# Kernel tuning notes

Measured on AMD Instinct MI355X. Metric: run time of the kernel, lower is better.

Reference implementation:

```python
import jax, jax.numpy as jnp
import numpy as np

N = 8192       # paired user/item batch
D_IN = 10000   # interaction-vector length
H = 1024       # hidden width
E = 128        # shared embedding dim


def setup_inputs() -> dict:
    key = jax.random.key(0)
    ks = jax.random.split(key, 10)
    g = 5.0 / 3.0  # tanh gain used by the torch init

    def xavier(k, shape):
        fan_in, fan_out = shape
        std = g * np.sqrt(2.0 / (fan_in + fan_out))
        return jax.random.normal(k, shape, dtype=jnp.float32) * std

    return {
        "user_data": jax.random.normal(ks[0], (N, D_IN), dtype=jnp.float32),
        "item_data": jax.random.normal(ks[1], (N, D_IN), dtype=jnp.float32),
        "Wu1": xavier(ks[2], (D_IN, H)),
        "bu1": jnp.full((H,), 0.01, dtype=jnp.float32),
        "Wu2": xavier(ks[3], (H, E)),
        "bu2": jnp.full((E,), 0.01, dtype=jnp.float32),
        "Wi1": xavier(ks[4], (D_IN, H)),
        "bi1": jnp.full((H,), 0.01, dtype=jnp.float32),
        "Wi2": xavier(ks[5], (H, E)),
        "bi2": jnp.full((E,), 0.01, dtype=jnp.float32),
    }


def reference(user_data, item_data, Wu1, bu1, Wu2, bu2, Wi1, bi1, Wi2, bi2):
    # Encoders (dropout is identity at inference). PolyLinear: Linear -> ReLU -> Linear.
    p = jax.nn.relu(user_data @ Wu1 + bu1) @ Wu2 + bu2   # [N, E]
    q = jax.nn.relu(item_data @ Wi1 + bi1) @ Wi2 + bi2   # [N, E]
    # (p @ q.T).diag() == row-wise dot product; identical math, O(N*E) not O(N^2*E).
    return jnp.einsum("ne,ne->n", p, q)
```

## Files before the change

### kernel.cpp

```cpp
#include <hip/hip_runtime.h>
#include <hip/hip_bf16.h>
#include <stdint.h>

#define KP   10112
#define DIN  10000
#define NB   8192
#define HID  1024
#define EMB  128
#define NKT  313
#define NI   79

typedef __attribute__((ext_vector_type(8))) __bf16 bf16x8;
typedef __attribute__((ext_vector_type(4))) float  f32x4;
typedef __attribute__((ext_vector_type(4))) unsigned short ushort4v;

typedef const __attribute__((address_space(1))) void* gas_cp;
typedef __attribute__((address_space(3))) void* las_p;

__device__ __forceinline__ unsigned short f2bf(float f) {
    union { float f; unsigned u; } c; c.f = f;
    unsigned u = c.u;
    u += 0x7FFFu + ((u >> 16) & 1u);
    return (unsigned short)(u >> 16);
}

__global__ void conv_pad(const float* __restrict__ src, unsigned short* __restrict__ dst) {
    const int c4  = blockIdx.x * blockDim.x + threadIdx.x;
    const int row = blockIdx.y;
    if (c4 >= KP / 4) return;
    ushort4v o;
    if (c4 < DIN / 4) {
        float4 a = *(const float4*)(src + (size_t)row * DIN + (size_t)c4 * 4);
        o[0] = f2bf(a.x); o[1] = f2bf(a.y); o[2] = f2bf(a.z); o[3] = f2bf(a.w);
    } else {
        o[0] = o[1] = o[2] = o[3] = 0;
    }
    *(ushort4v*)(dst + (size_t)row * KP + (size_t)c4 * 4) = o;
}

__global__ void conv_transpose(const float* __restrict__ src, unsigned short* __restrict__ dst,
                               int K, int N, int Kp) {
    __shared__ float tile[64][33];
    const int tx = threadIdx.x & 31, ty = threadIdx.x >> 5;
    const int k0 = blockIdx.x * 64, n0 = blockIdx.y * 32;
#pragma unroll
    for (int j = 0; j < 8; ++j) {
        int k = k0 + ty + j * 8;
        tile[ty + j * 8][tx] = (k < K) ? src[(size_t)k * N + n0 + tx] : 0.0f;
    }
    __syncthreads();
#pragma unroll
    for (int j = 0; j < 4; ++j) {
        int n = n0 + ty + j * 8;
        unsigned short lo = f2bf(tile[2 * tx][ty + j * 8]);
        unsigned short hi = f2bf(tile[2 * tx + 1][ty + j * 8]);
        unsigned int packed = (unsigned int)lo | ((unsigned int)hi << 16);
        *(unsigned int*)(dst + (size_t)n * Kp + k0 + 2 * tx) = packed;
    }
}

#define DSR(d, ad, off) asm volatile("ds_read_b128 %0, %1 offset:" off : "=v"(d) : "v"(ad))
#define GATE(n) do { asm volatile("s_waitcnt lgkmcnt(" #n ")" ::: "memory"); \
                     __builtin_amdgcn_sched_barrier(0); } while (0)

__global__ __launch_bounds__(512, 2)
void gemm1_4p(const unsigned short* __restrict__ Abf,
              const unsigned short* __restrict__ W1t,
              const float* __restrict__ b1u, const float* __restrict__ b1i,
              unsigned short* __restrict__ H1) {
    __shared__ __align__(16) unsigned short lds_[81920];

    const int t  = threadIdx.x;
    const int lane = t & 63, wv = t >> 6;
    const int wm = wv >> 2, wn = wv & 3;
    const int rA = lane & 15, kg = lane >> 4;

    const int side = blockIdx.x >> 2, bn = blockIdx.x & 3, bm = blockIdx.y;

    const unsigned short* AbfS = Abf + (size_t)side * NB * KP;
    const unsigned short* W1tS = W1t + (size_t)side * HID * KP;
    const float* bias = side ? b1i : b1u;
    unsigned short* Cout = H1 + (size_t)side * NB * HID;

    const int rowSA = bm * 256 + (t >> 3);
    const int rowSB = bn * 256 + (t >> 3);
    const int kcl   = ((t & 7) ^ ((t >> 3) & 7)) * 8;

    const int xk0 = ((0 * 4 + kg) ^ (rA & 7)) * 8;
    const int xk1 = ((1 * 4 + kg) ^ (rA & 7)) * 8;

    const unsigned ldsB = (unsigned)(size_t)lds_;
    const unsigned aC0 = ldsB + wm * 16384 + rA * 128 + xk0 * 2;
    const unsigned aC1 = ldsB + wm * 16384 + rA * 128 + xk1 * 2;
    const unsigned bC0 = ldsB + 98304 + (wn >> 1) * 16384 + (wn & 1) * 8192 + rA * 128 + xk0 * 2;
    const unsigned bC1 = ldsB + 98304 + (wn >> 1) * 16384 + (wn & 1) * 8192 + rA * 128 + xk1 * 2;

    f32x4 acc[8][4] = {};
    bf16x8 a[4][2], b[4][2];

    auto stA = [&](int tile, int h, int buf) {
        const unsigned short* s = AbfS + (size_t)(rowSA + h * 128) * KP + tile * 64 + kcl;
        __builtin_amdgcn_global_load_lds((gas_cp)s, (las_p)(lds_ + buf * 16384 + h * 8192 + wv * 512), 16, 0, 0);
        __builtin_amdgcn_global_load_lds((gas_cp)(s + (size_t)64 * KP), (las_p)(lds_ + buf * 16384 + h * 8192 + 4096 + wv * 512), 16, 0, 0);
    };
    auto stB = [&](int tile, int h, int par) {
        const unsigned short* s = W1tS + (size_t)(rowSB + h * 128) * KP + tile * 64 + kcl;
        __builtin_amdgcn_global_load_lds((gas_cp)s, (las_p)(lds_ + 49152 + par * 16384 + h * 8192 + wv * 512), 16, 0, 0);
        __builtin_amdgcn_global_load_lds((gas_cp)(s + (size_t)64 * KP), (las_p)(lds_ + 49152 + par * 16384 + h * 8192 + 4096 + wv * 512), 16, 0, 0);
    };

    auto rdB01 = [&](int par) {
        unsigned b0 = bC0 + par * 32768, b1 = bC1 + par * 32768;
        DSR(b[0][0], b0, "0");    DSR(b[0][1], b1, "0");
        DSR(b[1][0], b0, "2048"); DSR(b[1][1], b1, "2048");
    };
    auto rdB23 = [&](int par) {
        unsigned b0 = bC0 + par * 32768 + 4096, b1 = bC1 + par * 32768 + 4096;
        DSR(b[2][0], b0, "0");    DSR(b[2][1], b1, "0");
        DSR(b[3][0], b0, "2048"); DSR(b[3][1], b1, "2048");
    };
    auto rdA4 = [&](int buf, int mq) {
        unsigned a0 = aC0 + buf * 32768 + mq * 8192, a1 = aC1 + buf * 32768 + mq * 8192;
        DSR(a[0][0], a0, "0");    DSR(a[0][1], a1, "0");
        DSR(a[1][0], a0, "2048"); DSR(a[1][1], a1, "2048");
        DSR(a[2][0], a0, "4096"); DSR(a[2][1], a1, "4096");
        DSR(a[3][0], a0, "6144"); DSR(a[3][1], a1, "6144");
    };
    auto mmj = [&](int mq, int j, int nq) {
        acc[mq*4+j][nq*2+0] = __builtin_amdgcn_mfma_f32_16x16x32_bf16(a[j][0], b[nq*2+0][0], acc[mq*4+j][nq*2+0], 0, 0, 0);
        acc[mq*4+j][nq*2+0] = __builtin_amdgcn_mfma_f32_16x16x32_bf16(a[j][1], b[nq*2+0][1], acc[mq*4+j][nq*2+0], 0, 0, 0);
        acc[mq*4+j][nq*2+1] = __builtin_amdgcn_mfma_f32_16x16x32_bf16(a[j][0], b[nq*2+1][0], acc[mq*4+j][nq*2+1], 0, 0, 0);
        acc[mq*4+j][nq*2+1] = __builtin_amdgcn_mfma_f32_16x16x32_bf16(a[j][1], b[nq*2+1][1], acc[mq*4+j][nq*2+1], 0, 0, 0);
    };
    auto mmcol = [&](int mq, int col) {
#pragma unroll
        for (int j = 0; j < 4; ++j) {
            acc[mq*4+j][col] = __builtin_amdgcn_mfma_f32_16x16x32_bf16(a[j][0], b[col][0], acc[mq*4+j][col], 0, 0, 0);
            acc[mq*4+j][col] = __builtin_amdgcn_mfma_f32_16x16x32_bf16(a[j][1], b[col][1], acc[mq*4+j][col], 0, 0, 0);
        }
    };

    stA(0, 0, 0); stA(0, 1, 0);
    stB(0, 0, 0); stB(0, 1, 0);
    stA(1, 0, 1); stA(1, 1, 1);
    asm volatile("s_waitcnt vmcnt(4)" ::: "memory");
    __builtin_amdgcn_s_barrier();

    int cA0 = 0, cA1 = 1, nA = 2;
    for (int i = 0; i < NI - 1; ++i) {
        const int T1 = 2 * i + 1, S0 = 2 * i + 2, S1 = 2 * i + 3;
        rdB01(0); rdA4(cA0, 0); rdB23(0);
        stB(T1, 0, 1); stB(T1, 1, 1);
        __builtin_amdgcn_s_setprio(1);
        GATE(10); mmj(0,0,0); GATE(8); mmj(0,1,0); GATE(6); mmj(0,2,0);
        GATE(4);  mmj(0,3,0); GATE(2); mmcol(0,2); GATE(0); mmcol(0,3);
        __builtin_amdgcn_s_setprio(0);
        __builtin_amdgcn_s_barrier();
        rdA4(cA0, 1);
        stA(S0, 0, nA); stA(S0, 1, nA);
        __builtin_amdgcn_s_setprio(1);
        GATE(6); mmj(1,0,0); GATE(4); mmj(1,1,0); GATE(2); mmj(1,2,0);
        GATE(0); mmj(1,3,0); mmcol(1,2); mmcol(1,3);
        __builtin_amdgcn_s_setprio(0);
        asm volatile("s_waitcnt vmcnt(4)" ::: "memory");
        __builtin_amdgcn_s_barrier();
        rdB01(1); rdA4(cA1, 0); rdB23(1);
        stB(S0, 0, 0); stB(S0, 1, 0);
        __builtin_amdgcn_s_setprio(1);
        GATE(10); mmj(0,0,0); GATE(8); mmj(0,1,0); GATE(6); mmj(0,2,0);
        GATE(4);  mmj(0,3,0); GATE(2); mmcol(0,2); GATE(0); mmcol(0,3);
        __builtin_amdgcn_s_setprio(0);
        __builtin_amdgcn_s_barrier();
        rdA4(cA1, 1);
        stA(S1, 0, cA0); stA(S1, 1, cA0);
        __builtin_amdgcn_s_setprio(1);
        GATE(6); mmj(1,0,0); GATE(4); mmj(1,1,0); GATE(2); mmj(1,2,0);
        GATE(0); mmj(1,3,0); mmcol(1,2); mmcol(1,3);
        __builtin_amdgcn_s_setprio(0);
        asm volatile("s_waitcnt vmcnt(4)" ::: "memory");
        __builtin_amdgcn_s_barrier();
        int tmp = cA1; cA1 = cA0; cA0 = nA; nA = tmp;
    }
    {
        const int TL = 2 * NI - 1;
        rdB01(0); rdA4(cA0, 0); rdB23(0);
        stB(TL, 0, 1); stB(TL, 1, 1);
        __builtin_amdgcn_s_setprio(1);
        GATE(10); mmj(0,0,0); GATE(8); mmj(0,1,0); GATE(6); mmj(0,2,0);
        GATE(4);  mmj(0,3,0); GATE(2); mmcol(0,2); GATE(0); mmcol(0,3);
        __builtin_amdgcn_s_setprio(0);
        __builtin_amdgcn_s_barrier();
        rdA4(cA0, 1);
        __builtin_amdgcn_s_setprio(1);
        GATE(6); mmj(1,0,0); GATE(4); mmj(1,1,0); GATE(2); mmj(1,2,0);
        GATE(0); mmj(1,3,0); mmcol(1,2); mmcol(1,3);
        __builtin_amdgcn_s_setprio(0);
        asm volatile("s_waitcnt vmcnt(0)" ::: "memory");
        __builtin_amdgcn_s_barrier();
        rdB01(1); rdA4(cA1, 0); rdB23(1);
        __builtin_amdgcn_s_setprio(1);
        GATE(10); mmj(0,0,0); GATE(8); mmj(0,1,0); GATE(6); mmj(0,2,0);
        GATE(4);  mmj(0,3,0); GATE(2); mmcol(0,2); GATE(0); mmcol(0,3);
        __builtin_amdgcn_s_setprio(0);
        __builtin_amdgcn_s_barrier();
        rdA4(cA1, 1);
        __builtin_amdgcn_s_setprio(1);
        GATE(6); mmj(1,0,0); GATE(4); mmj(1,1,0); GATE(2); mmj(1,2,0);
        GATE(0); mmj(1,3,0); mmcol(1,2); mmcol(1,3);
        __builtin_amdgcn_s_setprio(0);
    }

    const int rowbase = bm * 256 + wm * 128 + kg * 4;
    const int colbase = bn * 256 + wn * 64 + rA;
#pragma unroll
    for (int ni = 0; ni < 4; ++ni) {
        const int col = colbase + ni * 16;
        const float bv = bias[col];
#pragma unroll
        for (int mi = 0; mi < 8; ++mi) {
#pragma unroll
            for (int rr = 0; rr < 4; ++rr) {
                float v = fmaxf(acc[mi][ni][rr] + bv, 0.0f);
                Cout[(size_t)(rowbase + mi * 16 + rr) * HID + col] = f2bf(v);
            }
        }
    }
}

__global__ __launch_bounds__(256, 4)
void gemm1_fused(const float* __restrict__ Au, const float* __restrict__ Ai,
                 const unsigned short* __restrict__ W1t,
                 const float* __restrict__ b1u, const float* __restrict__ b1i,
                 unsigned short* __restrict__ H1) {
    __shared__ unsigned short As[2 * 4096];
    __shared__ unsigned short Bs[2 * 4096];

    const int t = threadIdx.x, lane = t & 63, wave = t >> 6;
    const int wr = wave >> 1, wc = wave & 1, rA = lane & 15, kg = lane >> 4;

    const int id   = (blockIdx.z * gridDim.y + blockIdx.y) * 8 + blockIdx.x;
    const int pos  = (id & 7) * 128 + (id >> 3);
    const int side = pos >> 9;
    const int rr   = pos & 511;
    const int bm   = rr >> 3, bn = rr & 7;

    const float* Ap = side ? Ai : Au;
    const unsigned short* Bt = W1t + (size_t)side * HID * KP;
    const float* bias = side ? b1i : b1u;
    unsigned short* Cout = H1 + (size_t)side * NB * HID;

    const int arow = t >> 1;
    const float* gA = Ap + (size_t)(bm * 128 + arow) * DIN + (t & 1) * 16;
    const int aswz = (arow >> 1) & 3;
    const int aw0 = arow * 32 + ((((t & 1) * 2)     ^ aswz)) * 8;
    const int aw1 = arow * 32 + ((((t & 1) * 2 + 1) ^ aswz)) * 8;

    const int srcc = (t & 3) ^ ((t >> 3) & 3);
    const unsigned short* gB = Bt + (size_t)(bn * 128 + (t >> 2)) * KP + (size_t)srcc * 8;
    const int wst = wave * 512;

    f32x4 acc[4][4] = {};
    const int swz  = (rA >> 1) & 3;
    const int aoff = (wr * 64 + rA) * 32 + (kg ^ swz) * 8;
    const int boff = (wc * 64 + rA) * 32 + (kg ^ swz) * 8;

    float4 ar0, ar1, ar2, ar3;

    auto loadA = [&](int kt2) {
        const float* p = gA + (size_t)kt2 * 32;
        if (kt2 == NKT - 1 && (t & 1)) {
            ar0 = make_float4(0, 0, 0, 0); ar1 = ar0; ar2 = ar0; ar3 = ar0;
        } else {
            ar0 = *(const float4*)(p);
            ar1 = *(const float4*)(p + 4);
            ar2 = *(const float4*)(p + 8);
            ar3 = *(const float4*)(p + 12);
        }
    };
    auto writeA = [&](int buf) {
        bf16x8 v0, v1;
        v0[0] = (__bf16)ar0.x; v0[1] = (__bf16)ar0.y; v0[2] = (__bf16)ar0.z; v0[3] = (__bf16)ar0.w;
        v0[4] = (__bf16)ar1.x; v0[5] = (__bf16)ar1.y; v0[6] = (__bf16)ar1.z; v0[7] = (__bf16)ar1.w;
        v1[0] = (__bf16)ar2.x; v1[1] = (__bf16)ar2.y; v1[2] = (__bf16)ar2.z; v1[3] = (__bf16)ar2.w;
        v1[4] = (__bf16)ar3.x; v1[5] = (__bf16)ar3.y; v1[6] = (__bf16)ar3.z; v1[7] = (__bf16)ar3.w;
        *(bf16x8*)(As + buf * 4096 + aw0) = v0;
        *(bf16x8*)(As + buf * 4096 + aw1) = v1;
    };
    auto stageB = [&](int kt2) {
        const int bo = (kt2 & 1) * 4096;
        const unsigned short* p = gB + (size_t)kt2 * 32;
        __builtin_amdgcn_global_load_lds((gas_cp)p,                     (las_p)(Bs + bo + wst),        16, 0, 0);
        __builtin_amdgcn_global_load_lds((gas_cp)(p + (size_t)64 * KP), (las_p)(Bs + bo + wst + 2048), 16, 0, 0);
    };
    auto compute = [&](int buf) {
        const int ao = buf * 4096 + aoff, bo = buf * 4096 + boff;
        bf16x8 b0 = *(const bf16x8*)(Bs + bo);
        bf16x8 b1 = *(const bf16x8*)(Bs + bo + 512);
        bf16x8 b2 = *(const bf16x8*)(Bs + bo + 1024);
        bf16x8 b3 = *(const bf16x8*)(Bs + bo + 1536);
#pragma unroll
        for (int m = 0; m < 4; ++m) {
            bf16x8 av = *(const bf16x8*)(As + ao + m * 512);
            acc[m][0] = __builtin_amdgcn_mfma_f32_16x16x32_bf16(av, b0, acc[m][0], 0, 0, 0);
            acc[m][1] = __builtin_amdgcn_mfma_f32_16x16x32_bf16(av, b1, acc[m][1], 0, 0, 0);
            acc[m][2] = __builtin_amdgcn_mfma_f32_16x16x32_bf16(av, b2, acc[m][2], 0, 0, 0);
            acc[m][3] = __builtin_amdgcn_mfma_f32_16x16x32_bf16(av, b3, acc[m][3], 0, 0, 0);
        }
    };

    loadA(0);
    __builtin_amdgcn_sched_barrier(0);
    stageB(0);
    __builtin_amdgcn_sched_barrier(0);
    writeA(0);
    loadA(1);
    asm volatile("s_waitcnt lgkmcnt(0)" ::: "memory");
    __builtin_amdgcn_s_barrier();

    for (int kt = 0; kt < NKT - 2; ++kt) {
        asm volatile("s_waitcnt vmcnt(4)" ::: "memory");
        __builtin_amdgcn_s_barrier();
        writeA((kt + 1) & 1);
        __builtin_amdgcn_sched_barrier(0);
        stageB(kt + 1);
        __builtin_amdgcn_sched_barrier(0);
        loadA(kt + 2);
        compute(kt & 1);
        asm volatile("s_waitcnt lgkmcnt(0)" ::: "memory");
        __builtin_amdgcn_s_barrier();
    }
    asm volatile("s_waitcnt vmcnt(4)" ::: "memory");
    __builtin_amdgcn_s_barrier();
    writeA((NKT - 1) & 1);
    __builtin_amdgcn_sched_barrier(0);
    stageB(NKT - 1);
    compute((NKT - 2) & 1);
    asm volatile("s_waitcnt lgkmcnt(0)" ::: "memory");
    __builtin_amdgcn_s_barrier();
    asm volatile("s_waitcnt vmcnt(0)" ::: "memory");
    __builtin_amdgcn_s_barrier();
    compute((NKT - 1) & 1);

    const int rowbase = bm * 128 + wr * 64 + kg * 4;
    const int colbase = bn * 128 + wc * 64 + rA;
#pragma unroll
    for (int n = 0; n < 4; ++n) {
        const int col = colbase + n * 16;
        const float bv = bias[col];
#pragma unroll
        for (int m = 0; m < 4; ++m) {
#pragma unroll
            for (int r = 0; r < 4; ++r) {
                float v = fmaxf(acc[m][n][r] + bv, 0.0f);
                Cout[(size_t)(rowbase + m * 16 + r) * HID + col] = f2bf(v);
            }
        }
    }
}

__global__ __launch_bounds__(256, 2)
void gemm2k(const unsigned short* __restrict__ H1,
            const unsigned short* __restrict__ W2t,
            const float* __restrict__ b2u, const float* __restrict__ b2i,
            float* __restrict__ PQh) {
    __shared__ unsigned short As[3 * 4096];
    __shared__ unsigned short Bs[3 * 4096];

    const int t = threadIdx.x, lane = t & 63, wave = t >> 6;
    const int wr = wave >> 1, wc = wave & 1, rA = lane & 15, kg = lane >> 4;
    const int kh = blockIdx.x, bm = blockIdx.y, side = blockIdx.z;
    const int nk = 512 / 32;

    const unsigned short* A  = H1  + (size_t)side * NB * HID + kh * 512;
    const unsigned short* Bt = W2t + (size_t)side * EMB * HID + kh * 512;
    const float* bias = side ? b2i : b2u;
    float* Cout = PQh + (size_t)(kh * 2 + side) * NB * EMB;

    const int srcc = (t & 3) ^ ((t >> 3) & 3);
    const unsigned short* ga = A  + (size_t)(bm * 128 + (t >> 2)) * HID + (size_t)srcc * 8;
    const unsigned short* gb = Bt + (size_t)(t >> 2) * HID + (size_t)srcc * 8;
    const size_t aP = (size_t)64 * HID;

    f32x4 acc[4][4] = {};
    const int swz  = (rA >> 1) & 3;
    const int aoff = (wr * 64 + rA) * 32 + (kg ^ swz) * 8;
    const int boff = (wc * 64 + rA) * 32 + (kg ^ swz) * 8;
    const int wst  = wave * 512;

    auto stage = [&](int buf) {
        const int bo = buf << 12;
        __builtin_amdgcn_global_load_lds((gas_cp)(ga),      (las_p)(As + bo + wst),        16, 0, 0);
        __builtin_amdgcn_global_load_lds((gas_cp)(ga + aP), (las_p)(As + bo + wst + 2048), 16, 0, 0);
        __builtin_amdgcn_global_load_lds((gas_cp)(gb),      (las_p)(Bs + bo + wst),        16, 0, 0);
        __builtin_amdgcn_global_load_lds((gas_cp)(gb + aP), (las_p)(Bs + bo + wst + 2048), 16, 0, 0);
        ga += 32; gb += 32;
    };
    auto compute = [&](int buf) {
        const int bo = buf << 12;
        bf16x8 af[4], bfr[4];
#pragma unroll
        for (int m = 0; m < 4; ++m) af[m]  = *(const bf16x8*)(As + bo + aoff + m * 512);
#pragma unroll
        for (int n = 0; n < 4; ++n) bfr[n] = *(const bf16x8*)(Bs + bo + boff + n * 512);
#pragma unroll
        for (int m = 0; m < 4; ++m)
#pragma unroll
            for (int n = 0; n < 4; ++n)
                acc[m][n] = __builtin_amdgcn_mfma_f32_16x16x32_bf16(af[m], bfr[n], acc[m][n], 0, 0, 0);
    };

    stage(0); stage(1);
    int cur = 0;
    for (int kt = 0; kt < nk - 2; ++kt) {
        int pfb = cur + 2; if (pfb >= 3) pfb -= 3;
        stage(pfb);
        asm volatile("s_waitcnt vmcnt(8)" ::: "memory");
        __builtin_amdgcn_s_barrier();
        compute(cur);
        __builtin_amdgcn_s_barrier();
        cur = (cur + 1 == 3) ? 0 : cur + 1;
    }
    asm volatile("s_waitcnt vmcnt(4)" ::: "memory");
    __builtin_amdgcn_s_barrier();
    compute(cur);
    cur = (cur + 1 == 3) ? 0 : cur + 1;
    asm volatile("s_waitcnt vmcnt(0)" ::: "memory");
    __builtin_amdgcn_s_barrier();
    compute(cur);

    const int rowbase = bm * 128 + wr * 64 + kg * 4;
    const int colbase = wc * 64 + rA;
#pragma unroll
    for (int n = 0; n < 4; ++n) {
        const int col = colbase + n * 16;
        const float bv = (kh == 0) ? bias[col] : 0.0f;
#pragma unroll
        for (int m = 0; m < 4; ++m) {
#pragma unroll
            for (int r = 0; r < 4; ++r) {
                Cout[(size_t)(rowbase + m * 16 + r) * EMB + col] = acc[m][n][r] + bv;
            }
        }
    }
}

__global__ void rowdot4(const float* __restrict__ PQh, float* __restrict__ out, int n) {
    int gid = blockIdx.x * blockDim.x + threadIdx.x;
    int w = gid >> 6, lane = gid & 63;
    if (w >= n) return;
    const size_t C = (size_t)NB * EMB;
    const float2 p0 = ((const float2*)(PQh + 0 * C + (size_t)w * EMB))[lane];
    const float2 q0 = ((const float2*)(PQh + 1 * C + (size_t)w * EMB))[lane];
    const float2 p1 = ((const float2*)(PQh + 2 * C + (size_t)w * EMB))[lane];
    const float2 q1 = ((const float2*)(PQh + 3 * C + (size_t)w * EMB))[lane];
    const float px = p0.x + p1.x, py = p0.y + p1.y;
    const float qx = q0.x + q1.x, qy = q0.y + q1.y;
    float s = px * qx + py * qy;
#pragma unroll
    for (int off = 32; off; off >>= 1) s += __shfl_down(s, off);
    if (lane == 0) out[w] = s;
}

extern "C" void kernel_launch(void* const* d_in, const int* in_sizes, int n_in,
                              void* d_out, int out_size, void* d_ws, size_t ws_size,
                              hipStream_t stream) {
    const float* user = (const float*)d_in[0];
    const float* item = (const float*)d_in[1];
    const float* Wu1  = (const float*)d_in[2];
    const float* bu1  = (const float*)d_in[3];
    const float* Wu2  = (const float*)d_in[4];
    const float* bu2  = (const float*)d_in[5];
    const float* Wi1  = (const float*)d_in[6];
    const float* bi1  = (const float*)d_in[7];
    const float* Wi2  = (const float*)d_in[8];
    const float* bi2  = (const float*)d_in[9];
    float* out = (float*)d_out;

    char* ws = (char*)d_ws;
    size_t off = 0;
    auto alloc = [&](size_t bytes) {
        char* p = ws + off;
        off += (bytes + 255) & ~(size_t)255;
        return p;
    };

    unsigned short* W1t = (unsigned short*)alloc((size_t)2 * HID * KP * 2);
    unsigned short* W2t = (unsigned short*)alloc((size_t)2 * EMB * HID * 2);
    float* PQh = (float*)alloc((size_t)4 * NB * EMB * 4);
    unsigned short* H1 = (unsigned short*)alloc((size_t)2 * NB * HID * 2);

    const bool full = ws_size >= (off + (size_t)2 * NB * KP * 2 + (1u << 20));

    dim3 blk(256);
    conv_transpose<<<dim3(KP / 64, HID / 32), blk, 0, stream>>>(Wu1, W1t,                      DIN, HID, KP);
    conv_transpose<<<dim3(KP / 64, HID / 32), blk, 0, stream>>>(Wi1, W1t + (size_t)HID * KP,   DIN, HID, KP);
    conv_transpose<<<dim3(HID / 64, EMB / 32), blk, 0, stream>>>(Wu2, W2t,                     HID, EMB, HID);
    conv_transpose<<<dim3(HID / 64, EMB / 32), blk, 0, stream>>>(Wi2, W2t + (size_t)EMB * HID, HID, EMB, HID);

    if (full) {
        unsigned short* Abf = (unsigned short*)alloc((size_t)2 * NB * KP * 2);
        conv_pad<<<dim3((KP / 4 + 255) / 256, NB), blk, 0, stream>>>(user, Abf);
        conv_pad<<<dim3((KP / 4 + 255) / 256, NB), blk, 0, stream>>>(item, Abf + (size_t)NB * KP);
        gemm1_4p<<<dim3(8, 32), dim3(512), 0, stream>>>(Abf, W1t, bu1, bi1, H1);
    } else {
        gemm1_fused<<<dim3(8, 64, 2), blk, 0, stream>>>(user, item, W1t, bu1, bi1, H1);
    }
    gemm2k<<<dim3(2, 64, 2), blk, 0, stream>>>(H1, W2t, bu2, bi2, PQh);
    rowdot4<<<(NB * 64) / 256, blk, 0, stream>>>(PQh, out, NB);
}
```

Baseline: 493.4 us.

## Fuse fp32-to-bf16 activation conversion into the 256x256 GEMM1 pipeline

After: 807.4 us. +63.6%, slower.

```diff
diff --git a/kernel.cpp b/kernel.cpp
--- a/kernel.cpp
+++ b/kernel.cpp
@@ -7,12 +7,10 @@
 #define NB   8192
 #define HID  1024
 #define EMB  128
-#define NKT  313
 #define NI   79
 
 typedef __attribute__((ext_vector_type(8))) __bf16 bf16x8;
 typedef __attribute__((ext_vector_type(4))) float  f32x4;
-typedef __attribute__((ext_vector_type(4))) unsigned short ushort4v;
 
 typedef const __attribute__((address_space(1))) void* gas_cp;
 typedef __attribute__((address_space(3))) void* las_p;
@@ -22,20 +20,6 @@
     unsigned u = c.u;
     u += 0x7FFFu + ((u >> 16) & 1u);
     return (unsigned short)(u >> 16);
-}
-
-__global__ void conv_pad(const float* __restrict__ src, unsigned short* __restrict__ dst) {
-    const int c4  = blockIdx.x * blockDim.x + threadIdx.x;
-    const int row = blockIdx.y;
-    if (c4 >= KP / 4) return;
-    ushort4v o;
-    if (c4 < DIN / 4) {
-        float4 a = *(const float4*)(src + (size_t)row * DIN + (size_t)c4 * 4);
-        o[0] = f2bf(a.x); o[1] = f2bf(a.y); o[2] = f2bf(a.z); o[3] = f2bf(a.w);
-    } else {
-        o[0] = o[1] = o[2] = o[3] = 0;
-    }
-    *(ushort4v*)(dst + (size_t)row * KP + (size_t)c4 * 4) = o;
 }
 
 __global__ void conv_transpose(const float* __restrict__ src, unsigned short* __restrict__ dst,
@@ -62,12 +46,15 @@
 #define DSR(d, ad, off) asm volatile("ds_read_b128 %0, %1 offset:" off : "=v"(d) : "v"(ad))
 #define GATE(n) do { asm volatile("s_waitcnt lgkmcnt(" #n ")" ::: "memory"); \
                      __builtin_amdgcn_sched_barrier(0); } while (0)
+#define SB0() __builtin_amdgcn_sched_barrier(0)
+
+struct ARegs { float4 r0, r1, r2, r3; int ok; };
 
 __global__ __launch_bounds__(512, 2)
-void gemm1_4p(const unsigned short* __restrict__ Abf,
-              const unsigned short* __restrict__ W1t,
-              const float* __restrict__ b1u, const float* __restrict__ b1i,
-              unsigned short* __restrict__ H1) {
+void gemm1_4pf(const float* __restrict__ Au, const float* __restrict__ Ai,
+               const unsigned short* __restrict__ W1t,
+               const float* __restrict__ b1u, const float* __restrict__ b1i,
+               unsigned short* __restrict__ H1) {
     __shared__ __align__(16) unsigned short lds_[81920];
 
     const int t  = threadIdx.x;
@@ -77,12 +64,17 @@
 
     const int side = blockIdx.x >> 2, bn = blockIdx.x & 3, bm = blockIdx.y;
 
-    const unsigned short* AbfS = Abf + (size_t)side * NB * KP;
+    const float* Asrc = side ? Ai : Au;
     const unsigned short* W1tS = W1t + (size_t)side * HID * KP;
     const float* bias = side ? b1i : b1u;
     unsigned short* Cout = H1 + (size_t)side * NB * HID;
 
-    const int rowSA = bm * 256 + (t >> 3);
+    const int ar  = t >> 2;
+    const int ag0 = (t & 3) * 2;
+    const float* gA = Asrc + (size_t)(bm * 256 + ar) * DIN + (t & 3) * 16;
+    const int aw0 = ar * 64 + ((ag0       ^ (ar & 7)) * 8);
+    const int aw1 = ar * 64 + (((ag0 + 1) ^ (ar & 7)) * 8);
+
     const int rowSB = bn * 256 + (t >> 3);
     const int kcl   = ((t & 7) ^ ((t >> 3) & 7)) * 8;
 
@@ -97,11 +89,28 @@
 
     f32x4 acc[8][4] = {};
     bf16x8 a[4][2], b[4][2];
-
-    auto stA = [&](int tile, int h, int buf) {
-        const unsigned short* s = AbfS + (size_t)(rowSA + h * 128) * KP + tile * 64 + kcl;
-        __builtin_amdgcn_global_load_lds((gas_cp)s, (las_p)(lds_ + buf * 16384 + h * 8192 + wv * 512), 16, 0, 0);
-        __builtin_amdgcn_global_load_lds((gas_cp)(s + (size_t)64 * KP), (las_p)(lds_ + buf * 16384 + h * 8192 + 4096 + wv * 512), 16, 0, 0);
+    ARegs G0, G1, G2, G3;
+
+    auto ldA = [&](int tl, int h, ARegs& G) {
+        G.ok = (tl * 64 + (t & 3) * 16) < DIN;
+        const float* p = gA + (size_t)(h * 128) * DIN + (G.ok ? tl * 64 : 0);
+        G.r0 = *(const float4*)(p);
+        G.r1 = *(const float4*)(p + 4);
+        G.r2 = *(const float4*)(p + 8);
+        G.r3 = *(const float4*)(p + 12);
+    };
+    auto wrA = [&](int buf, int h, ARegs& G) {
+        const float4 z = make_float4(0.f, 0.f, 0.f, 0.f);
+        const float4 r0 = G.ok ? G.r0 : z, r1 = G.ok ? G.r1 : z;
+        const float4 r2 = G.ok ? G.r2 : z, r3 = G.ok ? G.r3 : z;
+        bf16x8 v0, v1;
+        v0[0] = (__bf16)r0.x; v0[1] = (__bf16)r0.y; v0[2] = (__bf16)r0.z; v0[3] = (__bf16)r0.w;
+        v0[4] = (__bf16)r1.x; v0[5] = (__bf16)r1.y; v0[6] = (__bf16)r1.z; v0[7] = (__bf16)r1.w;
+        v1[0] = (__bf16)r2.x; v1[1] = (__bf16)r2.y; v1[2] = (__bf16)r2.z; v1[3] = (__bf16)r2.w;
+        v1[4] = (__bf16)r3.x; v1[5] = (__bf16)r3.y; v1[6] = (__bf16)r3.z; v1[7] = (__bf16)r3.w;
+        unsigned short* d = lds_ + buf * 16384 + h * 8192;
+        *(bf16x8*)(d + aw0) = v0;
+        *(bf16x8*)(d + aw1) = v1;
     };
     auto stB = [&](int tile, int h, int par) {
         const unsigned short* s = W1tS + (size_t)(rowSB + h * 128) * KP + tile * 64 + kcl;
@@ -140,39 +149,58 @@
         }
     };
 
-    stA(0, 0, 0); stA(0, 1, 0);
+    ldA(0, 0, G0); ldA(0, 1, G1);
+    SB0();
     stB(0, 0, 0); stB(0, 1, 0);
-    stA(1, 0, 1); stA(1, 1, 1);
-    asm volatile("s_waitcnt vmcnt(4)" ::: "memory");
+    SB0();
+    ldA(1, 0, G2); ldA(1, 1, G3);
+    SB0();
+    wrA(0, 0, G0); wrA(0, 1, G1);
+    wrA(1, 0, G2); wrA(1, 1, G3);
+    SB0();
+    ldA(2, 0, G0); ldA(2, 1, G1);
+    asm volatile("s_waitcnt lgkmcnt(0)" ::: "memory");
     __builtin_amdgcn_s_barrier();
 
     int cA0 = 0, cA1 = 1, nA = 2;
     for (int i = 0; i < NI - 1; ++i) {
-        const int T1 = 2 * i + 1, S0 = 2 * i + 2, S1 = 2 * i + 3;
+        const int T1 = 2 * i + 1, SB_ = 2 * i + 2, S1 = 2 * i + 3, S0n = 2 * i + 4;
+        ldA(S1, 0, G2);
+        SB0();
+        stB(T1, 0, 1); stB(T1, 1, 1);
+        SB0();
         rdB01(0); rdA4(cA0, 0); rdB23(0);
-        stB(T1, 0, 1); stB(T1, 1, 1);
         __builtin_amdgcn_s_setprio(1);
         GATE(10); mmj(0,0,0); GATE(8); mmj(0,1,0); GATE(6); mmj(0,2,0);
         GATE(4);  mmj(0,3,0); GATE(2); mmcol(0,2); GATE(0); mmcol(0,3);
         __builtin_amdgcn_s_setprio(0);
         __builtin_amdgcn_s_barrier();
+        wrA(nA, 0, G0); wrA(nA, 1, G1);
+        SB0();
+        ldA(S1, 1, G3);
+        SB0();
         rdA4(cA0, 1);
-        stA(S0, 0, nA); stA(S0, 1, nA);
         __builtin_amdgcn_s_setprio(1);
         GATE(6); mmj(1,0,0); GATE(4); mmj(1,1,0); GATE(2); mmj(1,2,0);
         GATE(0); mmj(1,3,0); mmcol(1,2); mmcol(1,3);
         __builtin_amdgcn_s_setprio(0);
         asm volatile("s_waitcnt vmcnt(4)" ::: "memory");
         __builtin_amdgcn_s_barrier();
+        ldA(S0n, 0, G0);
+        SB0();
+        stB(SB_, 0, 0); stB(SB_, 1, 0);
+        SB0();
         rdB01(1); rdA4(cA1, 0); rdB23(1);
-        stB(S0, 0, 0); stB(S0, 1, 0);
         __builtin_amdgcn_s_setprio(1);
         GATE(10); mmj(0,0,0); GATE(8); mmj(0,1,0); GATE(6); mmj(0,2,0);
         GATE(4);  mmj(0,3,0); GATE(2); mmcol(0,2); GATE(0); mmcol(0,3);
         __builtin_amdgcn_s_setprio(0);
         __builtin_amdgcn_s_barrier();
+        wrA(cA0, 0, G2); wrA(cA0, 1, G3);
+        SB0();
+        ldA(S0n, 1, G1);
+        SB0();
         rdA4(cA1, 1);
-        stA(S1, 0, cA0); stA(S1, 1, cA0);
         __builtin_amdgcn_s_setprio(1);
         GATE(6); mmj(1,0,0); GATE(4); mmj(1,1,0); GATE(2); mmj(1,2,0);
         GATE(0); mmj(1,3,0); mmcol(1,2); mmcol(1,3);
@@ -183,8 +211,9 @@
     }
     {
         const int TL = 2 * NI - 1;
+        stB(TL, 0, 1); stB(TL, 1, 1);
+        SB0();
         rdB01(0); rdA4(cA0, 0); rdB23(0);
-        stB(TL, 0, 1); stB(TL, 1, 1);
         __builtin_amdgcn_s_setprio(1);
         GATE(10); mmj(0,0,0); GATE(8); mmj(0,1,0); GATE(6); mmj(0,2,0);
         GATE(4);  mmj(0,3,0); GATE(2); mmcol(0,2); GATE(0); mmcol(0,3);
@@ -222,137 +251,6 @@
             for (int rr = 0; rr < 4; ++rr) {
                 float v = fmaxf(acc[mi][ni][rr] + bv, 0.0f);
                 Cout[(size_t)(rowbase + mi * 16 + rr) * HID + col] = f2bf(v);
-            }
-        }
-    }
-}
-
-__global__ __launch_bounds__(256, 4)
-void gemm1_fused(const float* __restrict__ Au, const float* __restrict__ Ai,
-                 const unsigned short* __restrict__ W1t,
-                 const float* __restrict__ b1u, const float* __restrict__ b1i,
-                 unsigned short* __restrict__ H1) {
-    __shared__ unsigned short As[2 * 4096];
-    __shared__ unsigned short Bs[2 * 4096];
-
-    const int t = threadIdx.x, lane = t & 63, wave = t >> 6;
-    const int wr = wave >> 1, wc = wave & 1, rA = lane & 15, kg = lane >> 4;
-
-    const int id   = (blockIdx.z * gridDim.y + blockIdx.y) * 8 + blockIdx.x;
-    const int pos  = (id & 7) * 128 + (id >> 3);
-    const int side = pos >> 9;
-    const int rr   = pos & 511;
-    const int bm   = rr >> 3, bn = rr & 7;
-
-    const float* Ap = side ? Ai : Au;
-    const unsigned short* Bt = W1t + (size_t)side * HID * KP;
-    const float* bias = side ? b1i : b1u;
-    unsigned short* Cout = H1 + (size_t)side * NB * HID;
-
-    const int arow = t >> 1;
-    const float* gA = Ap + (size_t)(bm * 128 + arow) * DIN + (t & 1) * 16;
-    const int aswz = (arow >> 1) & 3;
-    const int aw0 = arow * 32 + ((((t & 1) * 2)     ^ aswz)) * 8;
-    const int aw1 = arow * 32 + ((((t & 1) * 2 + 1) ^ aswz)) * 8;
-
-    const int srcc = (t & 3) ^ ((t >> 3) & 3);
-    const unsigned short* gB = Bt + (size_t)(bn * 128 + (t >> 2)) * KP + (size_t)srcc * 8;
-    const int wst = wave * 512;
-
-    f32x4 acc[4][4] = {};
-    const int swz  = (rA >> 1) & 3;
-    const int aoff = (wr * 64 + rA) * 32 + (kg ^ swz) * 8;
-    const int boff = (wc * 64 + rA) * 32 + (kg ^ swz) * 8;
-
-    float4 ar0, ar1, ar2, ar3;
-
-    auto loadA = [&](int kt2) {
-        const float* p = gA + (size_t)kt2 * 32;
-        if (kt2 == NKT - 1 && (t & 1)) {
-            ar0 = make_float4(0, 0, 0, 0); ar1 = ar0; ar2 = ar0; ar3 = ar0;
-        } else {
-            ar0 = *(const float4*)(p);
-            ar1 = *(const float4*)(p + 4);
-            ar2 = *(const float4*)(p + 8);
-            ar3 = *(const float4*)(p + 12);
-        }
-    };
-    auto writeA = [&](int buf) {
-        bf16x8 v0, v1;
-        v0[0] = (__bf16)ar0.x; v0[1] = (__bf16)ar0.y; v0[2] = (__bf16)ar0.z; v0[3] = (__bf16)ar0.w;
-        v0[4] = (__bf16)ar1.x; v0[5] = (__bf16)ar1.y; v0[6] = (__bf16)ar1.z; v0[7] = (__bf16)ar1.w;
-        v1[0] = (__bf16)ar2.x; v1[1] = (__bf16)ar2.y; v1[2] = (__bf16)ar2.z; v1[3] = (__bf16)ar2.w;
-        v1[4] = (__bf16)ar3.x; v1[5] = (__bf16)ar3.y; v1[6] = (__bf16)ar3.z; v1[7] = (__bf16)ar3.w;
-        *(bf16x8*)(As + buf * 4096 + aw0) = v0;
-        *(bf16x8*)(As + buf * 4096 + aw1) = v1;
-    };
-    auto stageB = [&](int kt2) {
-        const int bo = (kt2 & 1) * 4096;
-        const unsigned short* p = gB + (size_t)kt2 * 32;
-        __builtin_amdgcn_global_load_lds((gas_cp)p,                     (las_p)(Bs + bo + wst),        16, 0, 0);
-        __builtin_amdgcn_global_load_lds((gas_cp)(p + (size_t)64 * KP), (las_p)(Bs + bo + wst + 2048), 16, 0, 0);
-    };
-    auto compute = [&](int buf) {
-        const int ao = buf * 4096 + aoff, bo = buf * 4096 + boff;
-        bf16x8 b0 = *(const bf16x8*)(Bs + bo);
-        bf16x8 b1 = *(const bf16x8*)(Bs + bo + 512);
-        bf16x8 b2 = *(const bf16x8*)(Bs + bo + 1024);
-        bf16x8 b3 = *(const bf16x8*)(Bs + bo + 1536);
-#pragma unroll
-        for (int m = 0; m < 4; ++m) {
-            bf16x8 av = *(const bf16x8*)(As + ao + m * 512);
-            acc[m][0] = __builtin_amdgcn_mfma_f32_16x16x32_bf16(av, b0, acc[m][0], 0, 0, 0);
-            acc[m][1] = __builtin_amdgcn_mfma_f32_16x16x32_bf16(av, b1, acc[m][1], 0, 0, 0);
-            acc[m][2] = __builtin_amdgcn_mfma_f32_16x16x32_bf16(av, b2, acc[m][2], 0, 0, 0);
-            acc[m][3] = __builtin_amdgcn_mfma_f32_16x16x32_bf16(av, b3, acc[m][3], 0, 0, 0);
-        }
-    };
-
-    loadA(0);
-    __builtin_amdgcn_sched_barrier(0);
-    stageB(0);
-    __builtin_amdgcn_sched_barrier(0);
-    writeA(0);
-    loadA(1);
-    asm volatile("s_waitcnt lgkmcnt(0)" ::: "memory");
-    __builtin_amdgcn_s_barrier();
-
-    for (int kt = 0; kt < NKT - 2; ++kt) {
-        asm volatile("s_waitcnt vmcnt(4)" ::: "memory");
-        __builtin_amdgcn_s_barrier();
-        writeA((kt + 1) & 1);
-        __builtin_amdgcn_sched_barrier(0);
-        stageB(kt + 1);
-        __builtin_amdgcn_sched_barrier(0);
-        loadA(kt + 2);
-        compute(kt & 1);
-        asm volatile("s_waitcnt lgkmcnt(0)" ::: "memory");
-        __builtin_amdgcn_s_barrier();
-    }
-    asm volatile("s_waitcnt vmcnt(4)" ::: "memory");
-    __builtin_amdgcn_s_barrier();
-    writeA((NKT - 1) & 1);
-    __builtin_amdgcn_sched_barrier(0);
-    stageB(NKT - 1);
-    compute((NKT - 2) & 1);
-    asm volatile("s_waitcnt lgkmcnt(0)" ::: "memory");
-    __builtin_amdgcn_s_barrier();
-    asm volatile("s_waitcnt vmcnt(0)" ::: "memory");
-    __builtin_amdgcn_s_barrier();
-    compute((NKT - 1) & 1);
-
-    const int rowbase = bm * 128 + wr * 64 + kg * 4;
-    const int colbase = bn * 128 + wc * 64 + rA;
-#pragma unroll
-    for (int n = 0; n < 4; ++n) {
-        const int col = colbase + n * 16;
-        const float bv = bias[col];
-#pragma unroll
-        for (int m = 0; m < 4; ++m) {
-#pragma unroll
-            for (int r = 0; r < 4; ++r) {
-                float v = fmaxf(acc[m][n][r] + bv, 0.0f);
-                Cout[(size_t)(rowbase + m * 16 + r) * HID + col] = f2bf(v);
             }
         }
     }
@@ -489,22 +387,13 @@
     float* PQh = (float*)alloc((size_t)4 * NB * EMB * 4);
     unsigned short* H1 = (unsigned short*)alloc((size_t)2 * NB * HID * 2);
 
-    const bool full = ws_size >= (off + (size_t)2 * NB * KP * 2 + (1u << 20));
-
     dim3 blk(256);
     conv_transpose<<<dim3(KP / 64, HID / 32), blk, 0, stream>>>(Wu1, W1t,                      DIN, HID, KP);
     conv_transpose<<<dim3(KP / 64, HID / 32), blk, 0, stream>>>(Wi1, W1t + (size_t)HID * KP,   DIN, HID, KP);
     conv_transpose<<<dim3(HID / 64, EMB / 32), blk, 0, stream>>>(Wu2, W2t,                     HID, EMB, HID);
     conv_transpose<<<dim3(HID / 64, EMB / 32), blk, 0, stream>>>(Wi2, W2t + (size_t)EMB * HID, HID, EMB, HID);
 
-    if (full) {
-        unsigned short* Abf = (unsigned short*)alloc((size_t)2 * NB * KP * 2);
-        conv_pad<<<dim3((KP / 4 + 255) / 256, NB), blk, 0, stream>>>(user, Abf);
-        conv_pad<<<dim3((KP / 4 + 255) / 256, NB), blk, 0, stream>>>(item, Abf + (size_t)NB * KP);
-        gemm1_4p<<<dim3(8, 32), dim3(512), 0, stream>>>(Abf, W1t, bu1, bi1, H1);
-    } else {
-        gemm1_fused<<<dim3(8, 64, 2), blk, 0, stream>>>(user, item, W1t, bu1, bi1, H1);
-    }
+    gemm1_4pf<<<dim3(8, 32), dim3(512), 0, stream>>>(user, item, W1t, bu1, bi1, H1);
     gemm2k<<<dim3(2, 64, 2), blk, 0, stream>>>(H1, W2t, bu2, bi2, PQh);
     rowdot4<<<(NB * 64) / 256, blk, 0, stream>>>(PQh, out, NB);
 }
```
